# Optimization experiments

Measured on AMD Instinct MI355X. Metric: run time of the kernel, lower is better.

Reference implementation:

```python
import jax, jax.numpy as jnp
import numpy as np
from jax import lax

K, D = 7, 2                      # kernel_size, dilation
PAD = (K - 1) * D                # = 12, matches init padding
B, CIN, COUT, L = 8, 128, 256, 4096


def _na_indices(L2, k, d):
    """NATTEN-style dilated 1D neighborhood: key positions + rel-pos-bias indices."""
    i = jnp.arange(L2)
    r, ii = i % d, i // d
    Lg = (L2 - r + d - 1) // d                       # dilation-group lengths
    start = jnp.clip(ii - k // 2, 0, Lg - k)         # clamped window start (in-group)
    t = jnp.arange(k)
    pos = r[:, None] + d * (start[:, None] + t[None, :])        # [L2,k] key positions
    bidx = start[:, None] + t[None, :] - ii[:, None] + (k - 1)  # [L2,k] rpb index in [0,2k-2]
    return pos, bidx


def setup_inputs() -> dict:
    key = jax.random.key(0)
    ks = jax.random.split(key, 11)
    s = 0.05
    return {
        "x": jax.random.normal(ks[0], (B, CIN, L), jnp.float32),
        "conv1_v": jax.random.normal(ks[1], (COUT, CIN, K), jnp.float32) * s,
        "conv1_g": jax.random.uniform(ks[2], (COUT,), jnp.float32, 0.5, 1.5),
        "conv1_b": jax.random.normal(ks[3], (COUT,), jnp.float32) * s,
        "qkv_w": jax.random.normal(ks[4], (3 * COUT, COUT), jnp.float32) * s,
        "qkv_b": jax.random.normal(ks[5], (3 * COUT,), jnp.float32) * s,
        "rpb": jax.random.normal(ks[6], (1, 2 * K - 1), jnp.float32) * s,
        "proj_w": jax.random.normal(ks[7], (COUT, COUT), jnp.float32) * s,
        "proj_b": jax.random.normal(ks[8], (COUT,), jnp.float32) * s,
        "ds_w": jax.random.normal(ks[9], (COUT, CIN, 1), jnp.float32) * s,
        "ds_b": jax.random.normal(ks[10], (COUT,), jnp.float32) * s,
    }


def reference(x, conv1_v, conv1_g, conv1_b, qkv_w, qkv_b, rpb, proj_w, proj_b, ds_w, ds_b):
    # weight_norm: w = g * v / ||v|| over (in_ch, kernel) per out channel
    vn = jnp.sqrt(jnp.sum(conv1_v * conv1_v, axis=(1, 2), keepdims=True))
    w1 = conv1_g[:, None, None] * conv1_v / vn
    out = lax.conv_general_dilated(x, w1, (1,), [(PAD, PAD)], rhs_dilation=(D,),
                                   dimension_numbers=("NCH", "OIH", "NCH"))
    out = out + conv1_b[None, :, None]
    out = jax.nn.relu(out[:, :, :-PAD])              # chomp1 + relu (dropout = eval identity)

    # left-pad then neighborhood attention on [B, L2, C]
    h = jnp.pad(out, ((0, 0), (0, 0), (PAD, 0))).transpose(0, 2, 1)
    L2 = h.shape[1]
    qkv = h @ qkv_w.T + qkv_b
    q, k_, v = jnp.split(qkv, 3, axis=-1)            # single head, head_dim = COUT
    pos, bidx = _na_indices(L2, K, D)
    kg = k_[:, pos, :]                               # [B, L2, K, C]
    vg = v[:, pos, :]
    scores = jnp.einsum("blc,blkc->blk", q * (COUT ** -0.5), kg) + rpb[0][bidx][None]
    attn = jax.nn.softmax(scores, axis=-1)
    o = jnp.einsum("blk,blkc->blc", attn, vg) @ proj_w.T + proj_b

    out = jax.nn.relu(o.transpose(0, 2, 1)[:, :, :-PAD])   # chomp2 + relu
    res = jnp.einsum("bcl,oc->bol", x, ds_w[:, :, 0]) + ds_b[None, :, None]
    return jax.nn.relu(out + res)
```

## Files before the change

### kernel.cpp

```cpp
#include <hip/hip_runtime.h>
#include <math.h>

#define KW 7
#define PADW 12
#define BATCH 8
#define CIN 128
#define COUT 256
#define LEN 4096
#define L2V 4108
#define NQKV 768
#define KCONV 896
#define PTILE 64

typedef unsigned short u16;
typedef short v8s __attribute__((ext_vector_type(8)));
typedef float v4f __attribute__((ext_vector_type(4)));

#define KEY3(r) ((((r) & 3) ^ (((r) >> 2) & 1)))

__device__ __forceinline__ u16 f2bf(float f) {
  unsigned int x = __float_as_uint(f);
  x += 0x7fffu + ((x >> 16) & 1u);
  return (u16)(x >> 16);
}
__device__ __forceinline__ float bf2f(u16 u) {
  return __uint_as_float(((unsigned int)u) << 16);
}

__device__ __forceinline__ void gll16(const void* g, void* l) {
  __builtin_amdgcn_global_load_lds(
      (const __attribute__((address_space(1))) void*)g,
      (__attribute__((address_space(3))) void*)l, 16, 0, 0);
}

#define MFMA16(ACC, AA, BB)                                                    \
  { _Pragma("unroll") for (int fi_ = 0; fi_ < 4; ++fi_)                        \
    _Pragma("unroll") for (int fj_ = 0; fj_ < 4; ++fj_)                        \
      ACC[fi_][fj_] = __builtin_amdgcn_mfma_f32_16x16x32_bf16(                 \
          AA[fi_], BB[fj_], ACC[fi_][fj_], 0, 0, 0); }

__global__ __launch_bounds__(256) void prep_wn(
    const float* __restrict__ v, const float* __restrict__ g,
    u16* __restrict__ wt)
{
  const int c = blockIdx.x;
  const float* vo = v + (size_t)c * (CIN * KW);
  float s = 0.f;
  for (int i = threadIdx.x; i < CIN * KW; i += 256) { float t = vo[i]; s += t * t; }
#pragma unroll
  for (int off = 1; off < 64; off <<= 1) s += __shfl_xor(s, off);
  __shared__ float red[4];
  if ((threadIdx.x & 63) == 0) red[threadIdx.x >> 6] = s;
  __syncthreads();
  const float tot = red[0] + red[1] + red[2] + red[3];
  const float scale = g[c] / sqrtf(tot);
  for (int i = threadIdx.x; i < CIN * KW; i += 256) {
    const int ci = i / 7, t = i - ci * 7;
    wt[((size_t)c * KW + t) * CIN + ci] = f2bf(vo[i] * scale);
  }
}

__global__ __launch_bounds__(256) void prep_cast(
    const float* __restrict__ qw, const float* __restrict__ pw,
    const float* __restrict__ dw, u16* __restrict__ qwb,
    u16* __restrict__ pwb, u16* __restrict__ dwb)
{
  const int i4 = (blockIdx.x * 256 + threadIdx.x) * 4;
  const float* src; u16* dst; int off;
  if (i4 < 196608)      { src = qw; dst = qwb; off = i4; }
  else if (i4 < 262144) { src = pw; dst = pwb; off = i4 - 196608; }
  else                  { src = dw; dst = dwb; off = i4 - 262144; }
  const float4 vv = *(const float4*)(src + off);
  *(ushort4*)(dst + off) = make_ushort4(f2bf(vv.x), f2bf(vv.y), f2bf(vv.z), f2bf(vv.w));
}

__global__ __launch_bounds__(256) void zero_fill(
    u16* __restrict__ xT, u16* __restrict__ qkv, const float* __restrict__ qb)
{
  const int idx = blockIdx.x * 256 + threadIdx.x;
  if (idx < BATCH * PADW * CIN) {
    const int b = idx / (PADW * CIN), r = idx - b * (PADW * CIN);
    xT[(size_t)b * L2V * CIN + r] = 0;
  } else {
    const int k = idx - BATCH * PADW * CIN;
    const int b = k / (PADW * NQKV), r2 = k - b * (PADW * NQKV);
    const int row = r2 / NQKV, n = r2 - row * NQKV;
    qkv[((size_t)b * L2V + row) * NQKV + n] = f2bf(qb[n]);
  }
}

__global__ __launch_bounds__(256) void xpose(const float* __restrict__ x, u16* __restrict__ xT)
{
  const int b = blockIdx.y, p0 = blockIdx.x * 64;
  const int tx = threadIdx.x & 15, ty = threadIdx.x >> 4;
  const int p = p0 + ty * 4;
  const float* xb = x + (size_t)b * CIN * LEN;
  u16* xTb = xT + (size_t)b * L2V * CIN + (size_t)(PADW + p) * CIN;
#pragma unroll
  for (int half = 0; half < 2; ++half) {
    const int ci0 = half * 64 + tx * 4;
    float r[4][4];
#pragma unroll
    for (int i = 0; i < 4; ++i)
      *(float4*)r[i] = *(const float4*)(xb + (size_t)(ci0 + i) * LEN + p);
#pragma unroll
    for (int j = 0; j < 4; ++j)
      *(ushort4*)(xTb + (size_t)j * CIN + ci0) =
          make_ushort4(f2bf(r[0][j]), f2bf(r[1][j]), f2bf(r[2][j]), f2bf(r[3][j]));
  }
}

__global__ __launch_bounds__(256, 2) void conv_qkv_fused(
    const u16* __restrict__ wt, const u16* __restrict__ xT,
    const float* __restrict__ c1b, const u16* __restrict__ qwb,
    const float* __restrict__ qb, u16* __restrict__ qkv)
{
  const int b = blockIdx.y;
  const int p0 = blockIdx.x * PTILE;
  const int tid = threadIdx.x;
  const int w = tid >> 6, lane = tid & 63;
  const int l15 = lane & 15, kg = lane >> 4;

  __shared__ u16 hA[PTILE * 256];
  __shared__ u16 sA[2][256 * 32];
  __shared__ u16 sB[2][PTILE * 32];

  const int arow = tid >> 2, ach = tid & 3;
  const int akey = KEY3(arow);

  const u16* xTb = xT + (size_t)b * L2V * CIN + (size_t)p0 * CIN;

  v4f acc[4][4];
#pragma unroll
  for (int i = 0; i < 4; ++i)
#pragma unroll
    for (int j = 0; j < 4; ++j) acc[i][j] = (v4f){0.f, 0.f, 0.f, 0.f};

  auto stage_conv = [&](int s, int buf) {
    const int t = s >> 2, ci0 = (s & 3) << 5;
#pragma unroll
    for (int i = 0; i < 4; ++i) {
      const int row = i * 64 + arow;
      gll16(wt + (size_t)row * KCONV + t * CIN + ci0 + ((ach ^ akey) << 3),
            (void*)&sA[buf][(i * 256 + tid) * 8]);
    }
    gll16(xTb + (size_t)(2 * t + arow) * CIN + ci0 + ((ach ^ akey) << 3),
          (void*)&sB[buf][tid * 8]);
  };

  stage_conv(0, 0);
  __syncthreads();
  for (int s = 0; s < 28; ++s) {
    const int buf = s & 1;
    if (s < 27) stage_conv(s + 1, buf ^ 1);
    v8s a[4], bb[4];
#pragma unroll
    for (int f = 0; f < 4; ++f) {
      const int c = w * 64 + f * 16 + l15;
      a[f] = *(const v8s*)&sA[buf][c * 32 + ((kg ^ KEY3(c)) << 3)];
      const int p = f * 16 + l15;
      bb[f] = *(const v8s*)&sB[buf][p * 32 + ((kg ^ KEY3(p)) << 3)];
    }
    MFMA16(acc, a, bb)
    __syncthreads();
  }

#pragma unroll
  for (int fi = 0; fi < 4; ++fi) {
    const int cb = w * 64 + fi * 16 + kg * 4;
    const float4 bv = *(const float4*)(c1b + cb);
    const int ch32 = cb >> 3, off = cb & 7;
#pragma unroll
    for (int fj = 0; fj < 4; ++fj) {
      const int p = fj * 16 + l15;
      *(ushort4*)&hA[p * 256 + ((ch32 ^ (p & 7)) << 3) + off] = make_ushort4(
          f2bf(fmaxf(acc[fi][fj][0] + bv.x, 0.f)),
          f2bf(fmaxf(acc[fi][fj][1] + bv.y, 0.f)),
          f2bf(fmaxf(acc[fi][fj][2] + bv.z, 0.f)),
          f2bf(fmaxf(acc[fi][fj][3] + bv.w, 0.f)));
      acc[fi][fj] = (v4f){0.f, 0.f, 0.f, 0.f};
    }
  }

  auto stage_qkv = [&](int st, int s, int buf) {
#pragma unroll
    for (int i = 0; i < 4; ++i) {
      const int row = i * 64 + arow;
      gll16(qwb + (size_t)(st * 256 + row) * COUT + (s << 5) + ((ach ^ akey) << 3),
            (void*)&sA[buf][(i * 256 + tid) * 8]);
    }
  };

  const size_t mg0 = (size_t)b * L2V + PADW + p0;
  for (int st = 0; st < 3; ++st) {
    stage_qkv(st, 0, 0);
    __syncthreads();
    for (int s = 0; s < 8; ++s) {
      const int buf = s & 1;
      if (s < 7) stage_qkv(st, s + 1, buf ^ 1);
      v8s a[4], bb[4];
#pragma unroll
      for (int f = 0; f < 4; ++f) {
        const int n = w * 64 + f * 16 + l15;
        a[f] = *(const v8s*)&sA[buf][n * 32 + ((kg ^ KEY3(n)) << 3)];
        const int p = f * 16 + l15;
        bb[f] = *(const v8s*)&hA[p * 256 + ((((s << 2) + kg) ^ (p & 7)) << 3)];
      }
      MFMA16(acc, a, bb)
      __syncthreads();
    }
    u16* T = &sA[0][0];
#pragma unroll
    for (int fi = 0; fi < 4; ++fi) {
      const int nl = fi * 16 + kg * 4;
      const float4 bv = *(const float4*)(qb + st * 256 + w * 64 + nl);
      const int nlc = nl >> 3, noff = nl & 7;
#pragma unroll
      for (int fj = 0; fj < 4; ++fj) {
        const int m = fj * 16 + l15;
        *(ushort4*)&T[w * 4096 + m * 64 + ((nlc ^ (m & 7)) << 3) + noff] = make_ushort4(
            f2bf(acc[fi][fj][0] + bv.x), f2bf(acc[fi][fj][1] + bv.y),
            f2bf(acc[fi][fj][2] + bv.z), f2bf(acc[fi][fj][3] + bv.w));
        acc[fi][fj] = (v4f){0.f, 0.f, 0.f, 0.f};
      }
    }
    __syncthreads();
    {
      const int m = tid >> 2, c0 = (tid & 3) << 1;
      u16* dst = qkv + (mg0 + m) * NQKV + st * 256;
#pragma unroll
      for (int q = 0; q < 4; ++q) {
        const int4 v0 = *(const int4*)&T[q * 4096 + m * 64 + (((c0 + 0) ^ (m & 7)) << 3)];
        const int4 v1 = *(const int4*)&T[q * 4096 + m * 64 + (((c0 + 1) ^ (m & 7)) << 3)];
        *(int4*)(dst + q * 64 + (c0 << 3)) = v0;
        *(int4*)(dst + q * 64 + (c0 << 3) + 8) = v1;
      }
    }
    __syncthreads();
  }
}

__global__ __launch_bounds__(256) void attn_bf16(
    const u16* __restrict__ qkv, const float* __restrict__ rpb,
    u16* __restrict__ ao)
{
  const int wid = (blockIdx.x << 2) + (threadIdx.x >> 6);
  const int lane = threadIdx.x & 63;
  const int b = wid >> 12;
  const int j = wid & 4095;
  const int r = j & 1, ii = j >> 1;
  int start = ii - 3;
  start = start < 0 ? 0 : start;
  start = start > 2047 ? 2047 : start;

  const u16* base = qkv + (size_t)b * L2V * NQKV;
  const ushort4 qv = *(const ushort4*)(base + (size_t)j * NQKV + 4 * lane);
  const float q0 = bf2f(qv.x) * 0.0625f, q1 = bf2f(qv.y) * 0.0625f;
  const float q2 = bf2f(qv.z) * 0.0625f, q3 = bf2f(qv.w) * 0.0625f;

  float sc[7];
  float mx = -1e30f;
#pragma unroll
  for (int t = 0; t < 7; ++t) {
    const int pos = r + 2 * (start + t);
    const ushort4 kv = *(const ushort4*)(base + (size_t)pos * NQKV + COUT + 4 * lane);
    float s = q0 * bf2f(kv.x) + q1 * bf2f(kv.y) + q2 * bf2f(kv.z) + q3 * bf2f(kv.w);
#pragma unroll
    for (int o = 1; o < 64; o <<= 1) s += __shfl_xor(s, o);
    s += rpb[start + t - ii + 6];
    sc[t] = s;
    mx = fmaxf(mx, s);
  }
  float sum = 0.f;
#pragma unroll
  for (int t = 0; t < 7; ++t) { sc[t] = __expf(sc[t] - mx); sum += sc[t]; }
  const float inv = 1.f / sum;

  float a0 = 0.f, a1 = 0.f, a2 = 0.f, a3 = 0.f;
#pragma unroll
  for (int t = 0; t < 7; ++t) {
    const int pos = r + 2 * (start + t);
    const ushort4 vv = *(const ushort4*)(base + (size_t)pos * NQKV + 2 * COUT + 4 * lane);
    const float wgt = sc[t] * inv;
    a0 += wgt * bf2f(vv.x); a1 += wgt * bf2f(vv.y);
    a2 += wgt * bf2f(vv.z); a3 += wgt * bf2f(vv.w);
  }
  *(ushort4*)(ao + ((size_t)(b * LEN + j)) * COUT + 4 * lane) =
      make_ushort4(f2bf(a0), f2bf(a1), f2bf(a2), f2bf(a3));
}

__global__ __launch_bounds__(256, 2) void projds_gll(
    const u16* __restrict__ ao, const u16* __restrict__ pwb,
    const float* __restrict__ pb, const u16* __restrict__ xT,
    const u16* __restrict__ dwb, const float* __restrict__ db,
    float* __restrict__ out)
{
  const int b = blockIdx.z;
  const int l0 = blockIdx.x * 128, o0 = blockIdx.y * 128;
  const int tid = threadIdx.x;
  const int w = tid >> 6, lane = tid & 63;
  const int l15 = lane & 15, kg = lane >> 4;
  const int wr = w >> 1, wc = w & 1;

  __shared__ u16 sX[2][128 * 32];
  __shared__ u16 sW[2][128 * 32];

  const int arow = tid >> 2, ach = tid & 3;
  const int akey = KEY3(arow);
  const u16* aob = ao + (size_t)b * LEN * COUT;
  const u16* xTb = xT + ((size_t)b * L2V + PADW) * CIN;

  auto stage1 = [&](int s, int buf) {
#pragma unroll
    for (int i = 0; i < 2; ++i) {
      const int row = i * 64 + arow;
      const int sl = (ach ^ akey) << 3;
      gll16(aob + (size_t)(l0 + row) * COUT + (s << 5) + sl,
            (void*)&sX[buf][(i * 256 + tid) * 8]);
      gll16(pwb + (size_t)(o0 + row) * COUT + (s << 5) + sl,
            (void*)&sW[buf][(i * 256 + tid) * 8]);
    }
  };
  auto stage2 = [&](int s, int buf) {
#pragma unroll
    for (int i = 0; i < 2; ++i) {
      const int row = i * 64 + arow;
      const int sl = (ach ^ akey) << 3;
      gll16(xTb + (size_t)(l0 + row) * CIN + (s << 5) + sl,
            (void*)&sX[buf][(i * 256 + tid) * 8]);
      gll16(dwb + (size_t)(o0 + row) * CIN + (s << 5) + sl,
            (void*)&sW[buf][(i * 256 + tid) * 8]);
    }
  };

  v4f acc[4][4];
#pragma unroll
  for (int i = 0; i < 4; ++i)
#pragma unroll
    for (int j = 0; j < 4; ++j) acc[i][j] = (v4f){0.f, 0.f, 0.f, 0.f};

  stage1(0, 0);
  __syncthreads();
  for (int ss = 0; ss < 12; ++ss) {
    const int buf = ss & 1;
    if (ss < 7) stage1(ss + 1, buf ^ 1);
    else if (ss < 11) stage2(ss - 7, buf ^ 1);
    v8s a[4], bb[4];
#pragma unroll
    for (int f = 0; f < 4; ++f) {
      const int lr = wr * 64 + f * 16 + l15;
      a[f] = *(const v8s*)&sX[buf][lr * 32 + ((kg ^ KEY3(lr)) << 3)];
      const int orr = wc * 64 + f * 16 + l15;
      bb[f] = *(const v8s*)&sW[buf][orr * 32 + ((kg ^ KEY3(orr)) << 3)];
    }
    MFMA16(acc, a, bb)
    if (ss == 7) {
#pragma unroll
      for (int fj = 0; fj < 4; ++fj) {
        const float pbv = pb[o0 + wc * 64 + fj * 16 + l15];
#pragma unroll
        for (int fi = 0; fi < 4; ++fi)
#pragma unroll
          for (int jj = 0; jj < 4; ++jj)
            acc[fi][fj][jj] = fmaxf(acc[fi][fj][jj] + pbv, 0.f);
      }
    }
    __syncthreads();
  }

  const int subl = kg;
#pragma unroll
  for (int fj = 0; fj < 4; ++fj) {
    const int o = o0 + wc * 64 + fj * 16 + l15;
    const float dbv = db[o];
    float* orow = out + ((size_t)(b * COUT + o)) * LEN;
#pragma unroll
    for (int fi = 0; fi < 4; ++fi) {
      const int lb = l0 + wr * 64 + fi * 16 + subl * 4;
      float v0 = acc[fi][fj][0] + dbv; v0 = v0 > 0.f ? v0 : 0.f;
      float v1 = acc[fi][fj][1] + dbv; v1 = v1 > 0.f ? v1 : 0.f;
      float v2 = acc[fi][fj][2] + dbv; v2 = v2 > 0.f ? v2 : 0.f;
      float v3 = acc[fi][fj][3] + dbv; v3 = v3 > 0.f ? v3 : 0.f;
      *(float4*)(orow + lb) = make_float4(v0, v1, v2, v3);
    }
  }
}

extern "C" void kernel_launch(void* const* d_in, const int* in_sizes, int n_in,
                              void* d_out, int out_size, void* d_ws, size_t ws_size,
                              hipStream_t stream)
{
  (void)in_sizes; (void)n_in; (void)out_size; (void)ws_size;
  const float* x   = (const float*)d_in[0];
  const float* c1v = (const float*)d_in[1];
  const float* c1g = (const float*)d_in[2];
  const float* c1b = (const float*)d_in[3];
  const float* qw  = (const float*)d_in[4];
  const float* qb  = (const float*)d_in[5];
  const float* rpb = (const float*)d_in[6];
  const float* pw  = (const float*)d_in[7];
  const float* pb  = (const float*)d_in[8];
  const float* dw  = (const float*)d_in[9];
  const float* db  = (const float*)d_in[10];
  float* out = (float*)d_out;

  char* ws = (char*)d_ws;
  u16* wt  = (u16*)(ws);
  u16* qwb = (u16*)(ws + 458752);
  u16* pwb = (u16*)(ws + 851968);
  u16* dwb = (u16*)(ws + 983040);
  u16* xT  = (u16*)(ws + 1048576);
  u16* qkv = (u16*)(ws + 26288128);
  u16* ao  = (u16*)(ws + 76767232);

  prep_wn<<<COUT, 256, 0, stream>>>(c1v, c1g, wt);
  prep_cast<<<288, 256, 0, stream>>>(qw, pw, dw, qwb, pwb, dwb);
  zero_fill<<<336, 256, 0, stream>>>(xT, qkv, qb);
  xpose<<<dim3(LEN / 64, BATCH), 256, 0, stream>>>(x, xT);
  conv_qkv_fused<<<dim3(LEN / PTILE, BATCH), 256, 0, stream>>>(wt, xT, c1b, qwb, qb, qkv);
  attn_bf16<<<(BATCH * LEN) / 4, 256, 0, stream>>>(qkv, rpb, ao);
  projds_gll<<<dim3(LEN / 128, COUT / 128, BATCH), 256, 0, stream>>>(ao, pwb, pb, xT, dwb, db, out);
}
```

Before: 110.0 us.

## Split conv_qkv_fused work across 8 waves with 512-thread blocks

Doubles the conv_qkv_fused block from 4 to 8 waves. Each wave now computes a 64x32 tile instead of 64x64, so it holds half the accumulators. Staging loads are spread over 512 threads, and the QKV epilogue is rebuilt to write through a 64x128 swizzled LDS transpose in two halves. The aim is more latency hiding and lower per-wave register pressure on the 512-block grid, at the cost of extra barriers and more redundant A-fragment LDS reads per MFMA.

```diff
diff --git a/kernel.cpp b/kernel.cpp
--- a/kernel.cpp
+++ b/kernel.cpp
@@ -33,9 +33,9 @@
       (__attribute__((address_space(3))) void*)l, 16, 0, 0);
 }
 
-#define MFMA16(ACC, AA, BB)                                                    \
+#define MFMA8(ACC, AA, BB)                                                     \
   { _Pragma("unroll") for (int fi_ = 0; fi_ < 4; ++fi_)                        \
-    _Pragma("unroll") for (int fj_ = 0; fj_ < 4; ++fj_)                        \
+    _Pragma("unroll") for (int fj_ = 0; fj_ < 2; ++fj_)                        \
       ACC[fi_][fj_] = __builtin_amdgcn_mfma_f32_16x16x32_bf16(                 \
           AA[fi_], BB[fj_], ACC[fi_][fj_], 0, 0, 0); }
 
@@ -110,7 +110,7 @@
   }
 }
 
-__global__ __launch_bounds__(256, 2) void conv_qkv_fused(
+__global__ __launch_bounds__(512, 4) void conv_qkv_fused(
     const u16* __restrict__ wt, const u16* __restrict__ xT,
     const float* __restrict__ c1b, const u16* __restrict__ qwb,
     const float* __restrict__ qb, u16* __restrict__ qkv)
@@ -120,32 +120,34 @@
   const int tid = threadIdx.x;
   const int w = tid >> 6, lane = tid & 63;
   const int l15 = lane & 15, kg = lane >> 4;
+  const int wA = w >> 1, wB = w & 1;
 
   __shared__ u16 hA[PTILE * 256];
   __shared__ u16 sA[2][256 * 32];
   __shared__ u16 sB[2][PTILE * 32];
 
-  const int arow = tid >> 2, ach = tid & 3;
-  const int akey = KEY3(arow);
-
   const u16* xTb = xT + (size_t)b * L2V * CIN + (size_t)p0 * CIN;
 
-  v4f acc[4][4];
+  v4f acc[4][2];
 #pragma unroll
   for (int i = 0; i < 4; ++i)
 #pragma unroll
-    for (int j = 0; j < 4; ++j) acc[i][j] = (v4f){0.f, 0.f, 0.f, 0.f};
+    for (int j = 0; j < 2; ++j) acc[i][j] = (v4f){0.f, 0.f, 0.f, 0.f};
 
   auto stage_conv = [&](int s, int buf) {
     const int t = s >> 2, ci0 = (s & 3) << 5;
 #pragma unroll
-    for (int i = 0; i < 4; ++i) {
-      const int row = i * 64 + arow;
-      gll16(wt + (size_t)row * KCONV + t * CIN + ci0 + ((ach ^ akey) << 3),
-            (void*)&sA[buf][(i * 256 + tid) * 8]);
-    }
-    gll16(xTb + (size_t)(2 * t + arow) * CIN + ci0 + ((ach ^ akey) << 3),
-          (void*)&sB[buf][tid * 8]);
+    for (int i = 0; i < 2; ++i) {
+      const int cidx = i * 512 + tid;
+      const int row = cidx >> 2, ch = cidx & 3;
+      gll16(wt + (size_t)row * KCONV + t * CIN + ci0 + ((ch ^ KEY3(row)) << 3),
+            (void*)&sA[buf][cidx * 8]);
+    }
+    if (tid < 256) {
+      const int row = tid >> 2, ch = tid & 3;
+      gll16(xTb + (size_t)(2 * t + row) * CIN + ci0 + ((ch ^ KEY3(row)) << 3),
+            (void*)&sB[buf][tid * 8]);
+    }
   };
 
   stage_conv(0, 0);
@@ -153,26 +155,29 @@
   for (int s = 0; s < 28; ++s) {
     const int buf = s & 1;
     if (s < 27) stage_conv(s + 1, buf ^ 1);
-    v8s a[4], bb[4];
+    v8s a[4], bb[2];
 #pragma unroll
     for (int f = 0; f < 4; ++f) {
-      const int c = w * 64 + f * 16 + l15;
+      const int c = wA * 64 + f * 16 + l15;
       a[f] = *(const v8s*)&sA[buf][c * 32 + ((kg ^ KEY3(c)) << 3)];
-      const int p = f * 16 + l15;
+    }
+#pragma unroll
+    for (int f = 0; f < 2; ++f) {
+      const int p = wB * 32 + f * 16 + l15;
       bb[f] = *(const v8s*)&sB[buf][p * 32 + ((kg ^ KEY3(p)) << 3)];
     }
-    MFMA16(acc, a, bb)
+    MFMA8(acc, a, bb)
     __syncthreads();
   }
 
 #pragma unroll
   for (int fi = 0; fi < 4; ++fi) {
-    const int cb = w * 64 + fi * 16 + kg * 4;
+    const int cb = wA * 64 + fi * 16 + kg * 4;
     const float4 bv = *(const float4*)(c1b + cb);
     const int ch32 = cb >> 3, off = cb & 7;
 #pragma unroll
-    for (int fj = 0; fj < 4; ++fj) {
-      const int p = fj * 16 + l15;
+    for (int fj = 0; fj < 2; ++fj) {
+      const int p = wB * 32 + fj * 16 + l15;
       *(ushort4*)&hA[p * 256 + ((ch32 ^ (p & 7)) << 3) + off] = make_ushort4(
           f2bf(fmaxf(acc[fi][fj][0] + bv.x, 0.f)),
           f2bf(fmaxf(acc[fi][fj][1] + bv.y, 0.f)),
@@ -184,10 +189,11 @@
 
   auto stage_qkv = [&](int st, int s, int buf) {
 #pragma unroll
-    for (int i = 0; i < 4; ++i) {
-      const int row = i * 64 + arow;
-      gll16(qwb + (size_t)(st * 256 + row) * COUT + (s << 5) + ((ach ^ akey) << 3),
-            (void*)&sA[buf][(i * 256 + tid) * 8]);
+    for (int i = 0; i < 2; ++i) {
+      const int cidx = i * 512 + tid;
+      const int row = cidx >> 2, ch = cidx & 3;
+      gll16(qwb + (size_t)(st * 256 + row) * COUT + (s << 5) + ((ch ^ KEY3(row)) << 3),
+            (void*)&sA[buf][cidx * 8]);
     }
   };
 
@@ -198,45 +204,49 @@
     for (int s = 0; s < 8; ++s) {
       const int buf = s & 1;
       if (s < 7) stage_qkv(st, s + 1, buf ^ 1);
-      v8s a[4], bb[4];
+      v8s a[4], bb[2];
 #pragma unroll
       for (int f = 0; f < 4; ++f) {
-        const int n = w * 64 + f * 16 + l15;
+        const int n = wA * 64 + f * 16 + l15;
         a[f] = *(const v8s*)&sA[buf][n * 32 + ((kg ^ KEY3(n)) << 3)];
-        const int p = f * 16 + l15;
-        bb[f] = *(const v8s*)&hA[p * 256 + ((((s << 2) + kg) ^ (p & 7)) << 3)];
       }
-      MFMA16(acc, a, bb)
+#pragma unroll
+      for (int f = 0; f < 2; ++f) {
+        const int m = wB * 32 + f * 16 + l15;
+        bb[f] = *(const v8s*)&hA[m * 256 + ((((s << 2) + kg) ^ (m & 7)) << 3)];
+      }
+      MFMA8(acc, a, bb)
       __syncthreads();
     }
     u16* T = &sA[0][0];
 #pragma unroll
-    for (int fi = 0; fi < 4; ++fi) {
-      const int nl = fi * 16 + kg * 4;
-      const float4 bv = *(const float4*)(qb + st * 256 + w * 64 + nl);
-      const int nlc = nl >> 3, noff = nl & 7;
-#pragma unroll
-      for (int fj = 0; fj < 4; ++fj) {
-        const int m = fj * 16 + l15;
-        *(ushort4*)&T[w * 4096 + m * 64 + ((nlc ^ (m & 7)) << 3) + noff] = make_ushort4(
-            f2bf(acc[fi][fj][0] + bv.x), f2bf(acc[fi][fj][1] + bv.y),
-            f2bf(acc[fi][fj][2] + bv.z), f2bf(acc[fi][fj][3] + bv.w));
-        acc[fi][fj] = (v4f){0.f, 0.f, 0.f, 0.f};
+    for (int h2 = 0; h2 < 2; ++h2) {
+#pragma unroll
+      for (int f1 = 0; f1 < 2; ++f1) {
+        const int fi = 2 * h2 + f1;
+        const int j = wA * 32 + f1 * 16 + kg * 4;
+        const int jc8 = j >> 3, noff = j & 7;
+        const float4 bv = *(const float4*)(qb + st * 256 + wA * 64 + h2 * 32 + f1 * 16 + kg * 4);
+#pragma unroll
+        for (int fj = 0; fj < 2; ++fj) {
+          const int m = wB * 32 + fj * 16 + l15;
+          *(ushort4*)&T[m * 128 + ((jc8 ^ (m & 15)) << 3) + noff] = make_ushort4(
+              f2bf(acc[fi][fj][0] + bv.x), f2bf(acc[fi][fj][1] + bv.y),
+              f2bf(acc[fi][fj][2] + bv.z), f2bf(acc[fi][fj][3] + bv.w));
+          acc[fi][fj] = (v4f){0.f, 0.f, 0.f, 0.f};
+        }
       }
-    }
-    __syncthreads();
-    {
-      const int m = tid >> 2, c0 = (tid & 3) << 1;
-      u16* dst = qkv + (mg0 + m) * NQKV + st * 256;
-#pragma unroll
-      for (int q = 0; q < 4; ++q) {
-        const int4 v0 = *(const int4*)&T[q * 4096 + m * 64 + (((c0 + 0) ^ (m & 7)) << 3)];
-        const int4 v1 = *(const int4*)&T[q * 4096 + m * 64 + (((c0 + 1) ^ (m & 7)) << 3)];
-        *(int4*)(dst + q * 64 + (c0 << 3)) = v0;
-        *(int4*)(dst + q * 64 + (c0 << 3) + 8) = v1;
+      __syncthreads();
+#pragma unroll
+      for (int i2 = 0; i2 < 2; ++i2) {
+        const int cidx = i2 * 512 + tid;
+        const int m = cidx >> 4, j16 = cidx & 15;
+        const int4 vv = *(const int4*)&T[m * 128 + ((j16 ^ (m & 15)) << 3)];
+        const int n = (j16 >> 2) * 64 + h2 * 32 + (j16 & 3) * 8;
+        *(int4*)(qkv + (mg0 + m) * NQKV + st * 256 + n) = vv;
       }
-    }
-    __syncthreads();
+      __syncthreads();
+    }
   }
 }
 
@@ -353,7 +363,12 @@
       const int orr = wc * 64 + f * 16 + l15;
       bb[f] = *(const v8s*)&sW[buf][orr * 32 + ((kg ^ KEY3(orr)) << 3)];
     }
-    MFMA16(acc, a, bb)
+#pragma unroll
+    for (int fi_ = 0; fi_ < 4; ++fi_)
+#pragma unroll
+      for (int fj_ = 0; fj_ < 4; ++fj_)
+        acc[fi_][fj_] = __builtin_amdgcn_mfma_f32_16x16x32_bf16(
+            a[fi_], bb[fj_], acc[fi_][fj_], 0, 0, 0);
     if (ss == 7) {
 #pragma unroll
       for (int fj = 0; fj < 4; ++fj) {
@@ -368,7 +383,6 @@
     __syncthreads();
   }
 
-  const int subl = kg;
 #pragma unroll
   for (int fj = 0; fj < 4; ++fj) {
     const int o = o0 + wc * 64 + fj * 16 + l15;
@@ -376,7 +390,7 @@
     float* orow = out + ((size_t)(b * COUT + o)) * LEN;
 #pragma unroll
     for (int fi = 0; fi < 4; ++fi) {
-      const int lb = l0 + wr * 64 + fi * 16 + subl * 4;
+      const int lb = l0 + wr * 64 + fi * 16 + kg * 4;
       float v0 = acc[fi][fj][0] + dbv; v0 = v0 > 0.f ? v0 : 0.f;
       float v1 = acc[fi][fj][1] + dbv; v1 = v1 > 0.f ? v1 : 0.f;
       float v2 = acc[fi][fj][2] + dbv; v2 = v2 > 0.f ? v2 : 0.f;
@@ -417,7 +431,7 @@
   prep_cast<<<288, 256, 0, stream>>>(qw, pw, dw, qwb, pwb, dwb);
   zero_fill<<<336, 256, 0, stream>>>(xT, qkv, qb);
   xpose<<<dim3(LEN / 64, BATCH), 256, 0, stream>>>(x, xT);
-  conv_qkv_fused<<<dim3(LEN / PTILE, BATCH), 256, 0, stream>>>(wt, xT, c1b, qwb, qb, qkv);
+  conv_qkv_fused<<<dim3(LEN / PTILE, BATCH), 512, 0, stream>>>(wt, xT, c1b, qwb, qb, qkv);
   attn_bf16<<<(BATCH * LEN) / 4, 256, 0, stream>>>(qkv, rpb, ao);
   projds_gll<<<dim3(LEN / 128, COUT / 128, BATCH), 256, 0, stream>>>(ao, pwb, pb, xT, dwb, db, out);
 }
```

Result: faster. 103.1 us (-6.2%).
